# Optimization experiments

Hardware: AMD Instinct MI355X
Metric: run time of the kernel (lower is better)

Reference implementation:

```python
import jax, jax.numpy as jnp
import numpy as np

D, H, T, P1, P2, B = 1024, 16, 2048, 16, 16, 2
HD = D // H
EPS = 1e-6
NEG = -1e30


def _ln(x, g, b):
    mu = jnp.mean(x, axis=-1, keepdims=True)
    var = jnp.mean((x - mu) ** 2, axis=-1, keepdims=True)
    return (x - mu) * jax.lax.rsqrt(var + EPS) * g + b


def _split_heads(x):  # [B,S,D] -> [B,H,S,HD]
    b, s, _ = x.shape
    return x.reshape(b, s, H, HD).transpose(0, 2, 1, 3)


def _merge_heads(x):  # [B,H,S,HD] -> [B,S,D]
    b, _, s, _ = x.shape
    return x.transpose(0, 2, 1, 3).reshape(b, s, D)


def setup_inputs() -> dict:
    key = jax.random.key(0)
    ks = jax.random.split(key, 24)
    s = 0.02
    inp = {
        'x': jax.random.normal(ks[0], (B, T, D), jnp.float32),
        'p1': jax.random.normal(ks[1], (B, P1, D), jnp.float32),
        'p2': jax.random.normal(ks[2], (B, P2, D), jnp.float32),
        'prior_1': jax.random.uniform(ks[3], (B, T), jnp.float32),
        'prior_2': jax.random.uniform(ks[4], (B, T), jnp.float32),
        'mask': jnp.ones((B, T), jnp.float32),
        'Wq': s * jax.random.normal(ks[5], (D, D), jnp.float32),
        'bq': jnp.zeros((D,), jnp.float32),
        'Wk': s * jax.random.normal(ks[6], (D, D), jnp.float32),
        'bk': jnp.zeros((D,), jnp.float32),
        'Wv': s * jax.random.normal(ks[7], (D, D), jnp.float32),
        'bv': jnp.zeros((D,), jnp.float32),
        'ln2_g': jnp.ones((D,), jnp.float32),
        'ln2_b': jnp.zeros((D,), jnp.float32),
        'W1': s * jax.random.normal(ks[8], (D, D), jnp.float32),
        'b1': jnp.zeros((D,), jnp.float32),
        'W2': s * jax.random.normal(ks[9], (D, D), jnp.float32),
        'b2': jnp.zeros((D,), jnp.float32),
        'Wp1': s * jax.random.normal(ks[10], (D, D), jnp.float32),
        'bp1': jnp.zeros((D,), jnp.float32),
        'Wp2': s * jax.random.normal(ks[11], (D, D), jnp.float32),
        'bp2': jnp.zeros((D,), jnp.float32),
    }
    return inp


def reference(x, p1, p2, prior_1, prior_2, mask, Wq, bq, Wk, bk, Wv, bv,
              ln2_g, ln2_b, W1, b1, W2, b2, Wp1, bp1, Wp2, bp2):
    scale = 1.0 / jnp.sqrt(jnp.asarray(HD, x.dtype))
    # Q/K are [proj(x); p1; p2] (prompts enter unprojected), V only from x.
    q = _split_heads(jnp.concatenate([x @ Wq + bq, p1, p2], axis=1))
    k = _split_heads(jnp.concatenate([x @ Wk + bk, p1, p2], axis=1))
    v = _split_heads(x @ Wv + bv)
    scores = jnp.einsum('bhqd,bhkd->bhqk', q, k) * scale  # [B,H,T+P,T+P]

    word = scores[:, :, :T, :T]                                  # [B,H,T,T]
    p1s = jnp.swapaxes(scores[:, :, :T, T:T + P1], -1, -2)       # [B,H,P1,T]
    p2s = jnp.swapaxes(scores[:, :, :T, T + P1:], -1, -2)        # [B,H,P2,T]

    word = word + (1.0 - mask)[:, None, None, :] * NEG           # mask_logits
    wa = jax.nn.softmax(word, axis=-1)
    p1a = jax.nn.softmax(jax.nn.softmax(p1s, axis=-1) * prior_1[:, None, None, :], axis=-1)
    p2a = jax.nn.softmax(jax.nn.softmax(p2s, axis=-1) * prior_2[:, None, None, :], axis=-1)

    ctx = jnp.einsum('bhqk,bhkd->bhqd', wa, v)    # [B,H,T,HD]
    p1_v = jnp.einsum('bhpk,bhkd->bhpd', p1a, ctx)
    p2_v = jnp.einsum('bhpk,bhkd->bhpd', p2a, ctx)

    residual = x + _merge_heads(ctx)
    out = _ln(residual, ln2_g, ln2_b)
    out = jax.nn.gelu(out @ W1 + b1, approximate=False)
    out = out @ W2 + b2 + residual

    p1_out = _ln(_merge_heads(p1_v) + p1, ln2_g, ln2_b)
    p1_out = jax.nn.gelu(p1_out @ Wp1 + bp1, approximate=False)

    p2_out = _ln(_merge_heads(p2_v) + p2, ln2_g, ln2_b)
    p2_out = jax.nn.gelu(p2_out @ Wp2 + bp2, approximate=False)
    return (out, p1_out, p2_out)
```

## Files before the change

kernel.cpp:

```cpp
#include <hip/hip_runtime.h>

#define DEV __device__ __forceinline__

typedef unsigned short u16;
typedef unsigned int   u32;
typedef short  s16x8  __attribute__((ext_vector_type(8)));
typedef float  f32x4  __attribute__((ext_vector_type(4)));
typedef float  f32x16 __attribute__((ext_vector_type(16)));

constexpr int Bc = 2, Hc = 16, Tc = 2048, Dc = 1024, HDc = 64, Mc = 4096;
constexpr int TP = Tc + 32;
constexpr float SCALEc = 0.125f;
constexpr float LOG2E = 1.44269504088896340736f;
constexpr float SCALE2c = SCALEc * LOG2E;
constexpr float NEGc = -1e30f;

typedef __attribute__((address_space(3))) void lds_void;
typedef const __attribute__((address_space(1))) void g_void;

DEV void gload16(const void* g, void* l) {
  __builtin_amdgcn_global_load_lds((g_void*)g, (lds_void*)l, 16, 0, 0);
}

DEV int swz(int r) { return (r & 7) ^ ((r >> 3) & 7); }

DEV u32 bfr(float f) {
  u32 u = __float_as_uint(f);
  return (u + 0x7fffu + ((u >> 16) & 1u)) >> 16;
}
DEV u32 cvtpk(float a, float b) {
  u32 r;
  asm("v_cvt_pk_bf16_f32 %0, %1, %2" : "=v"(r) : "v"(a), "v"(b));
  return r;
}
DEV s16x8 mk8(u32 w0, u32 w1, u32 w2, u32 w3) {
  union { u32 u[4]; s16x8 v; } x;
  x.u[0] = w0; x.u[1] = w1; x.u[2] = w2; x.u[3] = w3;
  return x.v;
}
DEV float geluf(float x) { return 0.5f * x * (1.0f + erff(x * 0.70710678118654752440f)); }

DEV float wredS(float v) {
  #pragma unroll
  for (int o = 32; o; o >>= 1) v += __shfl_xor(v, o);
  return v;
}
DEV float wredM(float v) {
  #pragma unroll
  for (int o = 32; o; o >>= 1) v = fmaxf(v, __shfl_xor(v, o));
  return v;
}
DEV float bredS(float v, float* sm) {
  v = wredS(v);
  __syncthreads();
  if ((threadIdx.x & 63) == 0) sm[threadIdx.x >> 6] = v;
  __syncthreads();
  return sm[0] + sm[1] + sm[2] + sm[3];
}
DEV float bredM(float v, float* sm) {
  v = wredM(v);
  __syncthreads();
  if ((threadIdx.x & 63) == 0) sm[threadIdx.x >> 6] = v;
  __syncthreads();
  return fmaxf(fmaxf(sm[0], sm[1]), fmaxf(sm[2], sm[3]));
}

__global__ __launch_bounds__(256) void transpose_w_k(const float* __restrict__ src,
                                                     u16* __restrict__ dst) {
  __shared__ float tile[32][33];
  int bx = blockIdx.x, by = blockIdx.y;
  int tx = threadIdx.x & 31, ty = threadIdx.x >> 5;
  #pragma unroll
  for (int i = 0; i < 32; i += 8)
    tile[ty + i][tx] = src[(size_t)(by * 32 + ty + i) * Dc + bx * 32 + tx];
  __syncthreads();
  #pragma unroll
  for (int i = 0; i < 32; i += 8)
    dst[(size_t)(bx * 32 + ty + i) * Dc + by * 32 + tx] = (u16)bfr(tile[tx][ty + i]);
}

__global__ __launch_bounds__(256) void cvt_bf16_k(const float* __restrict__ in,
                                                  u16* __restrict__ out, int n4) {
  int i = blockIdx.x * 256 + threadIdx.x;
  if (i < n4) {
    float4 v = ((const float4*)in)[i];
    ushort4 u;
    u.x = (u16)bfr(v.x); u.y = (u16)bfr(v.y); u.z = (u16)bfr(v.z); u.w = (u16)bfr(v.w);
    ((ushort4*)out)[i] = u;
  }
}

__global__ __launch_bounds__(256) void kprompt_k(const float* __restrict__ p1,
                                                 const float* __restrict__ p2,
                                                 u16* __restrict__ kb) {
  int i = blockIdx.x * 256 + threadIdx.x;
  int d = i & 63, j = (i >> 6) & 31, h = (i >> 11) & 15, b = i >> 15;
  float v = (j < 16) ? p1[(size_t)(b * 16 + j) * Dc + h * 64 + d]
                     : p2[(size_t)(b * 16 + j - 16) * Dc + h * 64 + d];
  kb[(((size_t)(b * Hc + h) * TP + Tc + j) << 6) + d] = (u16)bfr(v);
}

__global__ __launch_bounds__(256) void vtrans_k(const u16* __restrict__ vb,
                                                u16* __restrict__ vt) {
  __shared__ u16 tl[64][65];
  int bh = blockIdx.x >> 5, tc = blockIdx.x & 31;
  int d = threadIdx.x & 63, r = threadIdx.x >> 6;
  #pragma unroll
  for (int i = 0; i < 64; i += 4)
    tl[r + i][d] = vb[(((size_t)bh * Tc + tc * 64 + r + i) << 6) + d];
  __syncthreads();
  int t = threadIdx.x & 63, dd = threadIdx.x >> 6;
  #pragma unroll
  for (int i = 0; i < 64; i += 4)
    vt[((size_t)bh * 64 + dd + i) * Tc + tc * 64 + t] = tl[t][dd + i];
}

template <int MODE, int NBX>
__global__ __launch_bounds__(256, 3) void gemm128_k(
    const u16* __restrict__ A, const u16* __restrict__ Bt,
    const float* __restrict__ bias0, const float* __restrict__ bias1,
    const float* __restrict__ bias2,
    u16* __restrict__ outQ, u16* __restrict__ outK, u16* __restrict__ outV,
    u16* __restrict__ outB, float* __restrict__ outF,
    const float* __restrict__ resid) {
  __shared__ __align__(16) u16 as[2][128 * 32];
  __shared__ __align__(16) u16 bs[2][128 * 32];
  const int tid = threadIdx.x, lane = tid & 63, wave = tid >> 6;
  const int wr = wave >> 1, wc = wave & 1;
  const int nwg = gridDim.x, bid = (int)blockIdx.x;
  const int wg = (bid & 7) * (nwg >> 3) + (bid >> 3);
  const int row0 = (wg % NBX) * 128, col0 = (wg / NBX) * 128;

  f32x4 zero4;
  #pragma unroll
  for (int r = 0; r < 4; ++r) zero4[r] = 0.f;
  f32x4 acc[4][4];
  #pragma unroll
  for (int i = 0; i < 4; ++i)
    #pragma unroll
    for (int j = 0; j < 4; ++j) acc[i][j] = zero4;

  auto stage = [&](int buf, int kt) {
    const int k0 = kt * 32;
    #pragma unroll
    for (int is = 0; is < 2; ++is) {
      int q = is * 256 + tid; int r = q >> 2, c = q & 3, g = c ^ ((r >> 1) & 3);
      gload16(A + (size_t)(row0 + r) * Dc + k0 + g * 8,
              &as[buf][(is * 256 + wave * 64) * 8]);
    }
    #pragma unroll
    for (int is = 0; is < 2; ++is) {
      int q = is * 256 + tid; int r = q >> 2, c = q & 3, g = c ^ ((r >> 1) & 3);
      gload16(Bt + (size_t)(col0 + r) * Dc + k0 + g * 8,
              &bs[buf][(is * 256 + wave * 64) * 8]);
    }
  };

  stage(0, 0);
  asm volatile("s_waitcnt vmcnt(0)" ::: "memory");
  __syncthreads();

  int cur = 0;
  for (int kt = 0; kt < 32; ++kt) {
    if (kt + 1 < 32) stage(cur ^ 1, kt + 1);
    s16x8 af[4], bfv[4];
    #pragma unroll
    for (int f = 0; f < 4; ++f) {
      int r = wr * 64 + f * 16 + (lane & 15);
      int c = (lane >> 4) ^ ((r >> 1) & 3);
      af[f] = *(const s16x8*)&as[cur][r * 32 + c * 8];
    }
    #pragma unroll
    for (int f = 0; f < 4; ++f) {
      int r = wc * 64 + f * 16 + (lane & 15);
      int c = (lane >> 4) ^ ((r >> 1) & 3);
      bfv[f] = *(const s16x8*)&bs[cur][r * 32 + c * 8];
    }
    __builtin_amdgcn_s_setprio(1);
    #pragma unroll
    for (int i = 0; i < 4; ++i)
      #pragma unroll
      for (int j = 0; j < 4; ++j)
        acc[i][j] = __builtin_amdgcn_mfma_f32_16x16x32_bf16(af[i], bfv[j], acc[i][j], 0, 0, 0);
    __builtin_amdgcn_s_setprio(0);
    __syncthreads();
    cur ^= 1;
  }

  #pragma unroll
  for (int i = 0; i < 4; ++i) {
    #pragma unroll
    for (int j = 0; j < 4; ++j) {
      #pragma unroll
      for (int r = 0; r < 4; ++r) {
        int row = row0 + wr * 64 + i * 16 + (lane >> 4) * 4 + r;
        int col = col0 + wc * 64 + j * 16 + (lane & 15);
        float v = acc[i][j][r];
        if (MODE == 0) {
          int which = col >> 10, n = col & 1023;
          v += (which == 0 ? bias0 : (which == 1 ? bias1 : bias2))[n];
          int hh = n >> 6, d = n & 63, bb = row >> 11, t = row & 2047;
          u16 val = (u16)bfr(v);
          if (which == 0)      outQ[(((size_t)(bb * Hc + hh) * Tc + t) << 6) + d] = val;
          else if (which == 1) outK[(((size_t)(bb * Hc + hh) * TP + t) << 6) + d] = val;
          else                 outV[(((size_t)(bb * Hc + hh) * Tc + t) << 6) + d] = val;
        } else if (MODE == 1) {
          v = geluf(v + bias0[col]);
          outB[(size_t)row * Dc + col] = (u16)bfr(v);
        } else {
          outF[(size_t)row * Dc + col] = v + bias0[col] + resid[(size_t)row * Dc + col];
        }
      }
    }
  }
}

__global__ __launch_bounds__(256, 2) void attn_k(
    const u16* __restrict__ qb,
    const u16* __restrict__ kb,
    const u16* __restrict__ vt,
    const float* __restrict__ maskp,
    float* __restrict__ OP0, float* __restrict__ OP1,
    float* __restrict__ ML) {
  __shared__ __align__(16) u16 kls[2][64 * 64];
  __shared__ __align__(16) u16 vls[2][64 * 64];
  __shared__ float mls[1024];

  const int tid = threadIdx.x, lane = tid & 63, wave = tid >> 6;
  const int wg = ((int)blockIdx.x & 7) * 128 + ((int)blockIdx.x >> 3);
  const int ks = wg & 1, qt = (wg >> 1) & 15, bh = wg >> 5;
  const int b = bh >> 4;
  const int lo = lane & 31, h5 = lane >> 5;
  const size_t kbase = (size_t)bh * TP * 64;
  const size_t vbase = (size_t)bh * 64 * Tc;

  for (int i = tid; i < 1024; i += 256)
    mls[i] = (1.0f - maskp[(size_t)b * Tc + ks * 1024 + i]) * NEGc;

  const int q0 = qt * 128 + wave * 32;
  s16x8 qf[4];
  #pragma unroll
  for (int kc = 0; kc < 4; ++kc)
    qf[kc] = *(const s16x8*)(qb + ((size_t)bh * Tc + q0 + lo) * 64 + kc * 16 + h5 * 8);

  auto stageKV = [&](int buf, int kt2) {
    #pragma unroll
    for (int is = 0; is < 2; ++is) {
      int q = is * 256 + tid; int r = q >> 3, c = q & 7, g = c ^ swz(r);
      gload16(kb + kbase + (size_t)(kt2 * 64 + r) * 64 + g * 8,
              &kls[buf][(is * 256 + wave * 64) * 8]);
      gload16(vt + vbase + (size_t)r * Tc + kt2 * 64 + g * 8,
              &vls[buf][(is * 256 + wave * 64) * 8]);
    }
  };

  stageKV(0, ks * 16);
  asm volatile("s_waitcnt vmcnt(0)" ::: "memory");
  __syncthreads();

  f32x16 zero16;
  #pragma unroll
  for (int r = 0; r < 16; ++r) zero16[r] = 0.f;
  f32x16 O0 = zero16, O1 = zero16, racc = zero16;

  int cur = 0;
  for (int kt = 0; kt < 16; ++kt) {
    if (kt + 1 < 16) stageKV(cur ^ 1, ks * 16 + kt + 1);

    #pragma unroll
    for (int c = 0; c < 2; ++c) {
      f32x16 s = zero16;
      __builtin_amdgcn_s_setprio(1);
      #pragma unroll
      for (int kc = 0; kc < 4; ++kc) {
        int r = c * 32 + lo;
        int ci = (kc * 2 + h5) ^ swz(r);
        s16x8 kf = *(const s16x8*)&kls[cur][r * 64 + ci * 8];
        s = __builtin_amdgcn_mfma_f32_32x32x16_bf16(kf, qf[kc], s, 0, 0, 0);
      }
      __builtin_amdgcn_s_setprio(0);

      float4 mq[4];
      #pragma unroll
      for (int g = 0; g < 4; ++g)
        mq[g] = *(const float4*)&mls[kt * 64 + c * 32 + 4 * h5 + 8 * g];

      float p[16];
      #pragma unroll
      for (int r = 0; r < 16; ++r) {
        float mv = (&mq[r >> 2].x)[r & 3];
        p[r] = exp2f(s[r] * SCALE2c + mv);
        racc[r] += p[r];
      }

      #pragma unroll
      for (int k1 = 0; k1 < 2; ++k1) {
        u32 a01 = cvtpk(p[8 * k1 + 0], p[8 * k1 + 1]);
        u32 a23 = cvtpk(p[8 * k1 + 2], p[8 * k1 + 3]);
        u32 b01 = cvtpk(p[8 * k1 + 4], p[8 * k1 + 5]);
        u32 b23 = cvtpk(p[8 * k1 + 6], p[8 * k1 + 7]);
        u32 ax01 = (u32)__shfl_xor((int)a01, 32);
        u32 ax23 = (u32)__shfl_xor((int)a23, 32);
        u32 bx01 = (u32)__shfl_xor((int)b01, 32);
        u32 bx23 = (u32)__shfl_xor((int)b23, 32);
        u32 w0 = h5 ? bx01 : a01;
        u32 w1 = h5 ? bx23 : a23;
        u32 w2 = h5 ? b01 : ax01;
        u32 w3 = h5 ? b23 : ax23;
        s16x8 pf = mk8(w0, w1, w2, w3);
        __builtin_amdgcn_s_setprio(1);
        #pragma unroll
        for (int db = 0; db < 2; ++db) {
          int d = db * 32 + lo;
          int ci = (c * 4 + k1 * 2 + h5) ^ swz(d);
          s16x8 vf = *(const s16x8*)&vls[cur][d * 64 + ci * 8];
          if (db == 0) O0 = __builtin_amdgcn_mfma_f32_32x32x16_bf16(pf, vf, O0, 0, 0, 0);
          else         O1 = __builtin_amdgcn_mfma_f32_32x32x16_bf16(pf, vf, O1, 0, 0, 0);
        }
        __builtin_amdgcn_s_setprio(0);
      }
    }
    __syncthreads();
    cur ^= 1;
  }

  float* dst = ks ? OP1 : OP0;
  #pragma unroll
  for (int r = 0; r < 16; ++r) {
    int row = q0 + (r & 3) + 8 * (r >> 2) + 4 * h5;
    dst[((size_t)bh * Tc + row) * 64 + lo]      = O0[r];
    dst[((size_t)bh * Tc + row) * 64 + 32 + lo] = O1[r];
  }
  float lt = 0.f;
  #pragma unroll
  for (int r = 0; r < 16; ++r) lt += racc[r];
  lt += __shfl_xor(lt, 32);
  if (lane < 32)
    ML[((size_t)ks * 32 + bh) * Tc + q0 + lo] = lt;
}

__global__ __launch_bounds__(256) void combine_k(const float* __restrict__ OP0,
                                                 const float* __restrict__ OP1,
                                                 const float* __restrict__ ML,
                                                 float* __restrict__ ctx) {
  int idx = blockIdx.x * 256 + threadIdx.x;
  int row = idx >> 4;
  int c4 = (idx & 15) * 4;
  float linv = 1.0f / (ML[(size_t)row] + ML[(size_t)32 * Tc + row]);
  float4 v0 = *(const float4*)(OP0 + (size_t)row * 64 + c4);
  float4 v1 = *(const float4*)(OP1 + (size_t)row * 64 + c4);
  float4 o;
  o.x = (v0.x + v1.x) * linv;
  o.y = (v0.y + v1.y) * linv;
  o.z = (v0.z + v1.z) * linv;
  o.w = (v0.w + v1.w) * linv;
  *(float4*)(ctx + (size_t)row * 64 + c4) = o;
}

__global__ __launch_bounds__(256) void promptsc_k(const u16* __restrict__ qb,
                                                  const u16* __restrict__ kb,
                                                  float* __restrict__ SP) {
  __shared__ __align__(16) u16 kpls[32 * 64];
  const int tid = threadIdx.x, lane = tid & 63, wave = tid >> 6;
  const int qt = blockIdx.x, bh = blockIdx.y;
  const int lo = lane & 31, h5 = lane >> 5;
  const size_t kbase = (size_t)bh * TP * 64;

  {
    int r = tid >> 3, c = tid & 7, g = c ^ swz(r);
    gload16(kb + kbase + (size_t)(Tc + r) * 64 + g * 8, &kpls[wave * 64 * 8]);
  }
  const int q0 = qt * 128 + wave * 32;
  s16x8 qf[4];
  #pragma unroll
  for (int kc = 0; kc < 4; ++kc)
    qf[kc] = *(const s16x8*)(qb + ((size_t)bh * Tc + q0 + lo) * 64 + kc * 16 + h5 * 8);
  asm volatile("s_waitcnt vmcnt(0)" ::: "memory");
  __syncthreads();

  f32x16 sp;
  #pragma unroll
  for (int r = 0; r < 16; ++r) sp[r] = 0.f;
  #pragma unroll
  for (int kc = 0; kc < 4; ++kc) {
    int ci = (kc * 2 + h5) ^ swz(lo);
    s16x8 kf = *(const s16x8*)&kpls[lo * 64 + ci * 8];
    sp = __builtin_amdgcn_mfma_f32_32x32x16_bf16(kf, qf[kc], sp, 0, 0, 0);
  }
  #pragma unroll
  for (int r = 0; r < 16; ++r) {
    int pr = (r & 3) + 8 * (r >> 2) + 4 * h5;
    SP[((size_t)bh * 32 + pr) * Tc + q0 + lo] = sp[r] * SCALEc;
  }
}

__global__ __launch_bounds__(256) void prompt_softmax_k(float* __restrict__ SP,
                                                        const float* __restrict__ pr1,
                                                        const float* __restrict__ pr2) {
  __shared__ float sm[4];
  int row = blockIdx.x;
  int bh = row >> 5, p = row & 31, b = bh >> 4;
  const float* prior = (p < 16 ? pr1 : pr2) + (size_t)b * Tc;
  float* s = SP + (size_t)row * Tc;
  int tid = threadIdx.x;
  float v[8], pw[8];
  #pragma unroll
  for (int i = 0; i < 8; ++i) { int t = tid + i * 256; v[i] = s[t]; pw[i] = prior[t]; }
  float mx = -INFINITY;
  #pragma unroll
  for (int i = 0; i < 8; ++i) mx = fmaxf(mx, v[i]);
  mx = bredM(mx, sm);
  float sum = 0.f;
  #pragma unroll
  for (int i = 0; i < 8; ++i) { v[i] = __expf(v[i] - mx); sum += v[i]; }
  sum = bredS(sum, sm);
  float inv = 1.0f / sum;
  float mx2 = -INFINITY;
  #pragma unroll
  for (int i = 0; i < 8; ++i) { v[i] = v[i] * inv * pw[i]; mx2 = fmaxf(mx2, v[i]); }
  mx2 = bredM(mx2, sm);
  float sum2 = 0.f;
  #pragma unroll
  for (int i = 0; i < 8; ++i) { v[i] = __expf(v[i] - mx2); sum2 += v[i]; }
  sum2 = bredS(sum2, sm);
  float inv2 = 1.0f / sum2;
  #pragma unroll
  for (int i = 0; i < 8; ++i) s[tid + i * 256] = v[i] * inv2;
}

__global__ __launch_bounds__(256) void pv_partial_k(const float* __restrict__ PA,
                                                    const float* __restrict__ ctx,
                                                    float* __restrict__ PVP) {
  __shared__ float pal[32][128];
  const int bh = blockIdx.x, ts = blockIdx.y;
  const int tid = threadIdx.x;
  const int t0 = ts * 128;
  const float* pabase = PA + (size_t)bh * 32 * Tc;

  #pragma unroll
  for (int i = 0; i < 4; ++i) {
    int e = tid + i * 256;
    int p = e >> 5, c4 = e & 31;
    *(float4*)&pal[p][c4 * 4] = *(const float4*)&pabase[(size_t)p * Tc + t0 + c4 * 4];
  }
  __syncthreads();

  const int d4 = tid & 15, p0 = tid >> 4;
  const float* cb = ctx + ((size_t)bh * Tc + t0) * 64 + d4 * 4;
  float4 a0 = make_float4(0.f, 0.f, 0.f, 0.f);
  float4 a1 = make_float4(0.f, 0.f, 0.f, 0.f);
  for (int tt = 0; tt < 128; ++tt) {
    float4 v = *(const float4*)(cb + (size_t)tt * 64);
    float w0 = pal[p0][tt], w1 = pal[p0 + 16][tt];
    a0.x += w0 * v.x; a0.y += w0 * v.y; a0.z += w0 * v.z; a0.w += w0 * v.w;
    a1.x += w1 * v.x; a1.y += w1 * v.y; a1.z += w1 * v.z; a1.w += w1 * v.w;
  }
  float* o = PVP + (((size_t)ts * 32 + bh) * 32) * 64 + d4 * 4;
  *(float4*)(o + (size_t)p0 * 64) = a0;
  *(float4*)(o + (size_t)(p0 + 16) * 64) = a1;
}

__global__ __launch_bounds__(256) void pv_reduce_k(const float* __restrict__ PVP,
                                                   float* __restrict__ PVo) {
  int e = blockIdx.x * 256 + threadIdx.x;
  float s = 0.f;
  #pragma unroll
  for (int ts = 0; ts < 16; ++ts) s += PVP[(size_t)ts * 65536 + e];
  PVo[e] = s;
}

__global__ __launch_bounds__(256) void resln_k(const float* __restrict__ x,
                                               const float* __restrict__ ctx,
                                               const float* __restrict__ g,
                                               const float* __restrict__ be,
                                               float* __restrict__ res,
                                               u16* __restrict__ lnout) {
  __shared__ float sm[4];
  int row = blockIdx.x;
  int b = row >> 11, t = row & 2047;
  int tid = threadIdx.x, c4 = tid * 4;
  int h = c4 >> 6, d = c4 & 63;
  float4 xv = *(const float4*)(x + (size_t)row * Dc + c4);
  float4 cv = *(const float4*)(ctx + (((size_t)(b * Hc + h) * Tc + t) << 6) + d);
  float r0 = xv.x + cv.x, r1 = xv.y + cv.y, r2 = xv.z + cv.z, r3 = xv.w + cv.w;
  float4 rr; rr.x = r0; rr.y = r1; rr.z = r2; rr.w = r3;
  *(float4*)(res + (size_t)row * Dc + c4) = rr;
  float s = bredS(r0 + r1 + r2 + r3, sm);
  float sq = bredS(r0 * r0 + r1 * r1 + r2 * r2 + r3 * r3, sm);
  float mu = s * (1.0f / Dc);
  float var = sq * (1.0f / Dc) - mu * mu;
  float rs = rsqrtf(var + 1e-6f);
  ushort4 o;
  o.x = (u16)bfr((r0 - mu) * rs * g[c4 + 0] + be[c4 + 0]);
  o.y = (u16)bfr((r1 - mu) * rs * g[c4 + 1] + be[c4 + 1]);
  o.z = (u16)bfr((r2 - mu) * rs * g[c4 + 2] + be[c4 + 2]);
  o.w = (u16)bfr((r3 - mu) * rs * g[c4 + 3] + be[c4 + 3]);
  *(ushort4*)(lnout + (size_t)row * Dc + c4) = o;
}

__global__ __launch_bounds__(256) void promptln_k(const float* __restrict__ PVo,
                                                  const float* __restrict__ p1,
                                                  const float* __restrict__ p2,
                                                  const float* __restrict__ g,
                                                  const float* __restrict__ be,
                                                  float* __restrict__ PMLN) {
  __shared__ float sm[4];
  int row = blockIdx.x;
  int b = row >> 5, j = row & 31;
  int tid = threadIdx.x, c4 = tid * 4;
  int h = c4 >> 6, d = c4 & 63;
  const float* pr = (j < 16) ? (p1 + (size_t)(b * 16 + j) * Dc + c4)
                             : (p2 + (size_t)(b * 16 + j - 16) * Dc + c4);
  float4 pv4 = *(const float4*)(PVo + (((size_t)(b * Hc + h) * 32 + j) << 6) + d);
  float4 pp4 = *(const float4*)pr;
  float r0 = pv4.x + pp4.x, r1 = pv4.y + pp4.y, r2 = pv4.z + pp4.z, r3 = pv4.w + pp4.w;
  float s = bredS(r0 + r1 + r2 + r3, sm);
  float sq = bredS(r0 * r0 + r1 * r1 + r2 * r2 + r3 * r3, sm);
  float mu = s * (1.0f / Dc);
  float var = sq * (1.0f / Dc) - mu * mu;
  float rs = rsqrtf(var + 1e-6f);
  float4 o;
  o.x = (r0 - mu) * rs * g[c4 + 0] + be[c4 + 0];
  o.y = (r1 - mu) * rs * g[c4 + 1] + be[c4 + 1];
  o.z = (r2 - mu) * rs * g[c4 + 2] + be[c4 + 2];
  o.w = (r3 - mu) * rs * g[c4 + 3] + be[c4 + 3];
  *(float4*)(PMLN + (size_t)row * Dc + c4) = o;
}

__global__ __launch_bounds__(256) void pffn_partial_k(const float* __restrict__ PMLN,
                                                      const float* __restrict__ Wp1,
                                                      const float* __restrict__ Wp2,
                                                      float* __restrict__ PB) {
  __shared__ float pm[32][32];
  const int tid = threadIdx.x;
  const int ks = blockIdx.x, ct = blockIdx.y, s = blockIdx.z;
  const int c = ct * 256 + tid;
  const int k0 = ks * 32;
  const float* W = s ? Wp2 : Wp1;

  #pragma unroll
  for (int i = 0; i < 4; ++i) {
    int e = tid + i * 256;
    int r = e >> 5, kk = e & 31;
    int grow = (r >> 4) * 32 + s * 16 + (r & 15);
    pm[r][kk] = PMLN[(size_t)grow * Dc + k0 + kk];
  }
  __syncthreads();

  float acc[32];
  #pragma unroll
  for (int r = 0; r < 32; ++r) acc[r] = 0.f;
  for (int kk = 0; kk < 32; ++kk) {
    float w = W[(size_t)(k0 + kk) * Dc + c];
    #pragma unroll
    for (int r = 0; r < 32; ++r) acc[r] += pm[r][kk] * w;
  }

  float* pb = PB + (((size_t)ks * 2 + s) * 32) * Dc + c;
  #pragma unroll
  for (int r = 0; r < 32; ++r) pb[(size_t)r * Dc] = acc[r];
}

__global__ __launch_bounds__(256) void pffn_reduce_k(const float* __restrict__ PB,
                                                     const float* __restrict__ bp1,
                                                     const float* __restrict__ bp2,
                                                     float* __restrict__ out) {
  int e = blockIdx.x * 256 + threadIdx.x;
  int s = e >> 15, rem = e & 32767;
  int r = rem >> 10, c = rem & 1023;
  float sum = 0.f;
  const float* pb = PB + ((size_t)s * 32 + r) * Dc + c;
  #pragma unroll
  for (int ks = 0; ks < 32; ++ks) sum += pb[(size_t)ks * 2 * 32 * Dc];
  const float* bp = s ? bp2 : bp1;
  out[(size_t)Mc * Dc + (size_t)s * (32 * Dc) + (size_t)r * Dc + c] = geluf(sum + bp[c]);
}

extern "C" void kernel_launch(void* const* d_in, const int* in_sizes, int n_in,
                              void* d_out, int out_size, void* d_ws, size_t ws_size,
                              hipStream_t stream) {
  (void)in_sizes; (void)n_in; (void)out_size; (void)ws_size;
  const float* x   = (const float*)d_in[0];
  const float* p1  = (const float*)d_in[1];
  const float* p2  = (const float*)d_in[2];
  const float* pr1 = (const float*)d_in[3];
  const float* pr2 = (const float*)d_in[4];
  const float* msk = (const float*)d_in[5];
  const float* Wq  = (const float*)d_in[6];
  const float* bq  = (const float*)d_in[7];
  const float* Wk  = (const float*)d_in[8];
  const float* bk  = (const float*)d_in[9];
  const float* Wv  = (const float*)d_in[10];
  const float* bv  = (const float*)d_in[11];
  const float* g2  = (const float*)d_in[12];
  const float* be2 = (const float*)d_in[13];
  const float* W1  = (const float*)d_in[14];
  const float* b1  = (const float*)d_in[15];
  const float* W2  = (const float*)d_in[16];
  const float* b2  = (const float*)d_in[17];
  const float* Wp1 = (const float*)d_in[18];
  const float* bp1 = (const float*)d_in[19];
  const float* Wp2 = (const float*)d_in[20];
  const float* bp2 = (const float*)d_in[21];

  char* ws = (char*)d_ws;
  size_t off = 0;
  auto alloc = [&](size_t bytes) {
    void* p = ws + off;
    off += (bytes + 255) & ~(size_t)255;
    return p;
  };
  u16* WQKVT = (u16*)alloc((size_t)3072 * 1024 * 2);
  u16* W1T   = (u16*)alloc((size_t)1024 * 1024 * 2);
  u16* W2T   = (u16*)alloc((size_t)1024 * 1024 * 2);
  u16* XB    = (u16*)alloc((size_t)Mc * Dc * 2);
  u16* QB    = (u16*)alloc((size_t)32 * Tc * 64 * 2);
  u16* KB    = (u16*)alloc((size_t)32 * TP * 64 * 2);
  u16* VB    = (u16*)alloc((size_t)32 * Tc * 64 * 2);
  u16* VT    = (u16*)alloc((size_t)32 * 64 * Tc * 2);
  float* CTX = (float*)alloc((size_t)32 * Tc * 64 * 4);
  float* SP  = (float*)alloc((size_t)32 * 32 * Tc * 4);
  float* PVo = (float*)alloc((size_t)32 * 32 * 64 * 4);
  float* RES = (float*)alloc((size_t)Mc * Dc * 4);
  float* PMLN = (float*)alloc((size_t)64 * Dc * 4);
  float* ML  = (float*)alloc((size_t)2 * 32 * Tc * 4);
  float* PVP = (float*)alloc((size_t)16 * 32 * 32 * 64 * 4);
  u16* LNOUT = XB;
  u16* H1    = VB;
  float* PB  = SP;
  float* OP0 = CTX;
  float* OP1 = RES;

  float* outMain = (float*)d_out;

  transpose_w_k<<<dim3(32, 32), 256, 0, stream>>>(Wq, WQKVT);
  transpose_w_k<<<dim3(32, 32), 256, 0, stream>>>(Wk, WQKVT + (size_t)1024 * 1024);
  transpose_w_k<<<dim3(32, 32), 256, 0, stream>>>(Wv, WQKVT + (size_t)2 * 1024 * 1024);
  transpose_w_k<<<dim3(32, 32), 256, 0, stream>>>(W1, W1T);
  transpose_w_k<<<dim3(32, 32), 256, 0, stream>>>(W2, W2T);
  cvt_bf16_k<<<4096, 256, 0, stream>>>(x, XB, (Mc * Dc) / 4);
  gemm128_k<0, 32><<<768, 256, 0, stream>>>(XB, WQKVT, bq, bk, bv, QB, KB, VB,
                                            nullptr, nullptr, nullptr);
  kprompt_k<<<256, 256, 0, stream>>>(p1, p2, KB);
  vtrans_k<<<1024, 256, 0, stream>>>(VB, VT);
  attn_k<<<1024, 256, 0, stream>>>(QB, KB, VT, msk, OP0, OP1, ML);
  promptsc_k<<<dim3(16, 32), 256, 0, stream>>>(QB, KB, SP);
  combine_k<<<4096, 256, 0, stream>>>(OP0, OP1, ML, CTX);
  prompt_softmax_k<<<1024, 256, 0, stream>>>(SP, pr1, pr2);
  pv_partial_k<<<dim3(32, 16), 256, 0, stream>>>(SP, CTX, PVP);
  pv_reduce_k<<<256, 256, 0, stream>>>(PVP, PVo);
  resln_k<<<4096, 256, 0, stream>>>(x, CTX, g2, be2, RES, LNOUT);
  promptln_k<<<64, 256, 0, stream>>>(PVo, p1, p2, g2, be2, PMLN);
  pffn_partial_k<<<dim3(32, 4, 2), 256, 0, stream>>>(PMLN, Wp1, Wp2, PB);
  pffn_reduce_k<<<256, 256, 0, stream>>>(PB, bp1, bp2, outMain);
  gemm128_k<1, 32><<<256, 256, 0, stream>>>(LNOUT, W1T, b1, nullptr, nullptr,
                                            nullptr, nullptr, nullptr, H1,
                                            nullptr, nullptr);
  gemm128_k<2, 32><<<256, 256, 0, stream>>>(H1, W2T, b2, nullptr, nullptr,
                                            nullptr, nullptr, nullptr, nullptr,
                                            outMain, RES);
}
```

Before: 246.5 us.

## Stage GEMM epilogue through LDS for vector stores; use permlane32 swap in attention

New measurement: 236.6 us (median of 2 runs). -4.0%, faster.

```diff
diff --git a/kernel.cpp b/kernel.cpp
--- a/kernel.cpp
+++ b/kernel.cpp
@@ -123,8 +123,9 @@
     u16* __restrict__ outQ, u16* __restrict__ outK, u16* __restrict__ outV,
     u16* __restrict__ outB, float* __restrict__ outF,
     const float* __restrict__ resid) {
-  __shared__ __align__(16) u16 as[2][128 * 32];
-  __shared__ __align__(16) u16 bs[2][128 * 32];
+  __shared__ __align__(16) u16 smem[17408];
+  u16* as0 = smem;
+  u16* bs0 = smem + 2 * 128 * 32;
   const int tid = threadIdx.x, lane = tid & 63, wave = tid >> 6;
   const int wr = wave >> 1, wc = wave & 1;
   const int nwg = gridDim.x, bid = (int)blockIdx.x;
@@ -146,13 +147,13 @@
     for (int is = 0; is < 2; ++is) {
       int q = is * 256 + tid; int r = q >> 2, c = q & 3, g = c ^ ((r >> 1) & 3);
       gload16(A + (size_t)(row0 + r) * Dc + k0 + g * 8,
-              &as[buf][(is * 256 + wave * 64) * 8]);
+              as0 + (size_t)buf * 4096 + (is * 256 + wave * 64) * 8);
     }
     #pragma unroll
     for (int is = 0; is < 2; ++is) {
       int q = is * 256 + tid; int r = q >> 2, c = q & 3, g = c ^ ((r >> 1) & 3);
       gload16(Bt + (size_t)(col0 + r) * Dc + k0 + g * 8,
-              &bs[buf][(is * 256 + wave * 64) * 8]);
+              bs0 + (size_t)buf * 4096 + (is * 256 + wave * 64) * 8);
     }
   };
 
@@ -168,13 +169,13 @@
     for (int f = 0; f < 4; ++f) {
       int r = wr * 64 + f * 16 + (lane & 15);
       int c = (lane >> 4) ^ ((r >> 1) & 3);
-      af[f] = *(const s16x8*)&as[cur][r * 32 + c * 8];
+      af[f] = *(const s16x8*)&as0[cur * 4096 + r * 32 + c * 8];
     }
     #pragma unroll
     for (int f = 0; f < 4; ++f) {
       int r = wc * 64 + f * 16 + (lane & 15);
       int c = (lane >> 4) ^ ((r >> 1) & 3);
-      bfv[f] = *(const s16x8*)&bs[cur][r * 32 + c * 8];
+      bfv[f] = *(const s16x8*)&bs0[cur * 4096 + r * 32 + c * 8];
     }
     __builtin_amdgcn_s_setprio(1);
     #pragma unroll
@@ -187,30 +188,82 @@
     cur ^= 1;
   }
 
-  #pragma unroll
-  for (int i = 0; i < 4; ++i) {
-    #pragma unroll
-    for (int j = 0; j < 4; ++j) {
+  if (MODE == 0 || MODE == 1) {
+    const int CS = 136;
+    u16* ct = smem;
+    #pragma unroll
+    for (int i = 0; i < 4; ++i)
       #pragma unroll
-      for (int r = 0; r < 4; ++r) {
-        int row = row0 + wr * 64 + i * 16 + (lane >> 4) * 4 + r;
-        int col = col0 + wc * 64 + j * 16 + (lane & 15);
-        float v = acc[i][j][r];
-        if (MODE == 0) {
-          int which = col >> 10, n = col & 1023;
-          v += (which == 0 ? bias0 : (which == 1 ? bias1 : bias2))[n];
-          int hh = n >> 6, d = n & 63, bb = row >> 11, t = row & 2047;
-          u16 val = (u16)bfr(v);
-          if (which == 0)      outQ[(((size_t)(bb * Hc + hh) * Tc + t) << 6) + d] = val;
-          else if (which == 1) outK[(((size_t)(bb * Hc + hh) * TP + t) << 6) + d] = val;
-          else                 outV[(((size_t)(bb * Hc + hh) * Tc + t) << 6) + d] = val;
-        } else if (MODE == 1) {
-          v = geluf(v + bias0[col]);
-          outB[(size_t)row * Dc + col] = (u16)bfr(v);
-        } else {
-          outF[(size_t)row * Dc + col] = v + bias0[col] + resid[(size_t)row * Dc + col];
+      for (int j = 0; j < 4; ++j)
+        #pragma unroll
+        for (int r = 0; r < 4; ++r) {
+          int rl = wr * 64 + i * 16 + (lane >> 4) * 4 + r;
+          int cl = wc * 64 + j * 16 + (lane & 15);
+          float v = acc[i][j][r];
+          if (MODE == 0) {
+            int n = (col0 + cl) & 1023;
+            int which = (col0 + cl) >> 10;
+            v += (which == 0 ? bias0 : (which == 1 ? bias1 : bias2))[n];
+          } else {
+            v = geluf(v + bias0[col0 + cl]);
+          }
+          ct[rl * CS + cl] = (u16)bfr(v);
         }
+    __syncthreads();
+    #pragma unroll
+    for (int it = 0; it < 16; ++it) {
+      int linear = it * 256 + tid;
+      int row = linear >> 5, c4 = (linear & 31) * 4;
+      ushort4 val = *(const ushort4*)&ct[row * CS + c4];
+      int grow = row0 + row;
+      if (MODE == 1) {
+        *(ushort4*)&outB[(size_t)grow * Dc + col0 + c4] = val;
+      } else {
+        int col = col0 + c4;
+        int which = col >> 10, n = col & 1023;
+        int hh = n >> 6, d = n & 63, bb = grow >> 11, t = grow & 2047;
+        if (which == 0)
+          *(ushort4*)&outQ[(((size_t)(bb * Hc + hh) * Tc + t) << 6) + d] = val;
+        else if (which == 1)
+          *(ushort4*)&outK[(((size_t)(bb * Hc + hh) * TP + t) << 6) + d] = val;
+        else
+          *(ushort4*)&outV[(((size_t)(bb * Hc + hh) * Tc + t) << 6) + d] = val;
       }
+    }
+  } else {
+    const int CSF = 132;
+    float* cf = (float*)smem;
+    #pragma unroll
+    for (int p = 0; p < 2; ++p) {
+      if (wr == p) {
+        #pragma unroll
+        for (int i = 0; i < 4; ++i)
+          #pragma unroll
+          for (int j = 0; j < 4; ++j)
+            #pragma unroll
+            for (int r = 0; r < 4; ++r) {
+              int rl = i * 16 + (lane >> 4) * 4 + r;
+              int cl = wc * 64 + j * 16 + (lane & 15);
+              cf[rl * CSF + cl] = acc[i][j][r];
+            }
+      }
+      __syncthreads();
+      #pragma unroll
+      for (int it = 0; it < 8; ++it) {
+        int linear = it * 256 + tid;
+        int row = linear >> 5, c4 = (linear & 31) * 4;
+        float4 v = *(const float4*)&cf[row * CSF + c4];
+        int grow = row0 + p * 64 + row;
+        int col = col0 + c4;
+        float4 rr = *(const float4*)&resid[(size_t)grow * Dc + col];
+        float4 o;
+        o.x = v.x + bias0[col + 0] + rr.x;
+        o.y = v.y + bias0[col + 1] + rr.y;
+        o.z = v.z + bias0[col + 2] + rr.z;
+        o.w = v.w + bias0[col + 3] + rr.w;
+        *(float4*)&outF[(size_t)grow * Dc + col] = o;
+      }
+      __syncthreads();
     }
   }
 }
@@ -295,18 +348,12 @@
 
       #pragma unroll
       for (int k1 = 0; k1 < 2; ++k1) {
-        u32 a01 = cvtpk(p[8 * k1 + 0], p[8 * k1 + 1]);
-        u32 a23 = cvtpk(p[8 * k1 + 2], p[8 * k1 + 3]);
-        u32 b01 = cvtpk(p[8 * k1 + 4], p[8 * k1 + 5]);
-        u32 b23 = cvtpk(p[8 * k1 + 6], p[8 * k1 + 7]);
-        u32 ax01 = (u32)__shfl_xor((int)a01, 32);
-        u32 ax23 = (u32)__shfl_xor((int)a23, 32);
-        u32 bx01 = (u32)__shfl_xor((int)b01, 32);
-        u32 bx23 = (u32)__shfl_xor((int)b23, 32);
-        u32 w0 = h5 ? bx01 : a01;
-        u32 w1 = h5 ? bx23 : a23;
-        u32 w2 = h5 ? b01 : ax01;
-        u32 w3 = h5 ? b23 : ax23;
+        u32 w0 = cvtpk(p[8 * k1 + 0], p[8 * k1 + 1]);
+        u32 w1 = cvtpk(p[8 * k1 + 2], p[8 * k1 + 3]);
+        u32 w2 = cvtpk(p[8 * k1 + 4], p[8 * k1 + 5]);
+        u32 w3 = cvtpk(p[8 * k1 + 6], p[8 * k1 + 7]);
+        asm volatile("v_permlane32_swap_b32 %0, %1" : "+v"(w2), "+v"(w0));
+        asm volatile("v_permlane32_swap_b32 %0, %1" : "+v"(w3), "+v"(w1));
         s16x8 pf = mk8(w0, w1, w2, w3);
         __builtin_amdgcn_s_setprio(1);
         #pragma unroll
```
